# Kernel tuning notes

Measured on AMD Instinct MI355X. Metric: run time of the kernel, lower is better.

Reference implementation:

```python
import jax, jax.numpy as jnp
import numpy as np

B, C, H, W = 8, 256, 48, 48

def setup_inputs() -> dict:
    key = jax.random.key(0)
    ks = jax.random.split(key, 8)
    s = 1.0 / np.sqrt(C)  # conv2d default init scale (uniform fan_in)
    x = jax.random.normal(ks[0], (B, C, H, W), dtype=jnp.float32)
    y = jax.random.normal(ks[1], (B, C, H, W), dtype=jnp.float32)
    Wq = jax.random.uniform(ks[2], (C, C), jnp.float32, -s, s)
    bq = jax.random.uniform(ks[3], (C,), jnp.float32, -s, s)
    Wk = jax.random.uniform(ks[4], (C, C), jnp.float32, -s, s)
    bk = jax.random.uniform(ks[5], (C,), jnp.float32, -s, s)
    Wv = jax.random.uniform(ks[6], (C, C), jnp.float32, -s, s)
    bv = jax.random.uniform(ks[7], (C,), jnp.float32, -s, s)
    return {"x": x, "y": y, "Wq": Wq, "bq": bq, "Wk": Wk, "bk": bk, "Wv": Wv, "bv": bv}

def reference(x, y, Wq, bq, Wk, bk, Wv, bv):
    b, c, h, w = x.shape
    n = h * w
    # [B,C,H,W] -> tokens [B,N,C]
    xt = x.reshape(b, c, n).transpose(0, 2, 1)
    yt = y.reshape(b, c, n).transpose(0, 2, 1)
    # 1x1 convs == per-token linear projections
    q = xt @ Wq.T + bq  # [B,N,C]
    k = yt @ Wk.T + bk  # [B,N,C]
    v = yt @ Wv.T + bv  # [B,N,C]
    # unscaled QK^T softmax (module applies no 1/sqrt(d) scaling)
    scores = jnp.einsum('bnc,bmc->bnm', q, k)  # [B,N,N]
    attn = jax.nn.softmax(scores, axis=-1)
    out = jnp.einsum('bnm,bmc->bnc', attn, v)  # [B,N,C]
    return out.transpose(0, 2, 1).reshape(b, c, h, w)
```

## Files before the change

### kernel.cpp

```cpp
#include <hip/hip_runtime.h>
#include <stdint.h>

#define Bb 8
#define Cc 256
#define Nn 2304
#define PJT 18
#define QT 18
#define KSPLIT 3
#define TPS 24
#define L2E 1.44269504088896f
#define DEFER_THR 8.0f

#define AS1 __attribute__((address_space(1)))
#define AS3 __attribute__((address_space(3)))

typedef unsigned short u16;
typedef unsigned int u32;
typedef _Float16 h16;
typedef h16  h16x8 __attribute__((ext_vector_type(8)));
typedef u16  u16x8 __attribute__((ext_vector_type(8)));
typedef u16  u16x4 __attribute__((ext_vector_type(4)));
typedef u32  u32x4 __attribute__((ext_vector_type(4)));
typedef float f32x4 __attribute__((ext_vector_type(4)));
typedef float f32x2 __attribute__((ext_vector_type(2)));

static __device__ __forceinline__ u16 f2h(float f) {
  return __builtin_bit_cast(u16, (h16)f);
}
static __device__ __forceinline__ float h2f(u16 v) {
  return (float)__builtin_bit_cast(h16, v);
}
static __device__ __forceinline__ h16x8 ash(u16x8 v) {
  return __builtin_bit_cast(h16x8, v);
}
static __device__ __forceinline__ f32x4 mfma16(u16x8 a, u16x8 b, f32x4 c) {
  return __builtin_amdgcn_mfma_f32_16x16x32_f16(ash(a), ash(b), c, 0, 0, 0);
}
static __device__ __forceinline__ u32 pkf16(float a, float b) {
  return __builtin_bit_cast(u32, __builtin_amdgcn_cvt_pkrtz(a, b));
}

__global__ void prep_kernel(const float* __restrict__ Wq,
                            const float* __restrict__ Wk,
                            const float* __restrict__ Wv,
                            u16* __restrict__ Wf)
{
  const int tid = blockIdx.x * 256 + threadIdx.x;
  const int m   = tid >> 13;
  const int off = (tid & 8191) * 8;
  const float* src = (m == 0) ? Wq : (m == 1) ? Wk : Wv;
  const f32x4 a = *(const f32x4*)(src + off);
  const f32x4 c = *(const f32x4*)(src + off + 4);
  u16x8 o;
#pragma unroll
  for (int j = 0; j < 4; ++j) { o[j] = f2h(a[j]); o[j + 4] = f2h(c[j]); }
  *(u16x8*)(Wf + (size_t)m * 65536 + off) = o;
}

__global__ __launch_bounds__(256, 2) void proj_kernel(
    const float* __restrict__ x, const float* __restrict__ y,
    const u16* __restrict__ Wf,
    const float* __restrict__ bq, const float* __restrict__ bk,
    const float* __restrict__ bv,
    u16* __restrict__ Qf, u16* __restrict__ Kf, u16* __restrict__ Vf)
{
  __shared__ u16 sW[2][64 * 256];
  const int t    = threadIdx.x;
  const int b    = blockIdx.x;
  const int q0   = blockIdx.y * 128;
  const int z    = blockIdx.z;
  const int lane = t & 63;
  const int w    = t >> 6;
  const int quad = lane >> 4;
  const int l15  = lane & 15;

  const u16* WZ = Wf + (size_t)z * 65536;

  const int rbase = 2 * w + (lane >> 5);
  const int wcol  = ((lane & 31) ^ rbase) << 3;

  auto stage = [&](int rg, int buf) {
#pragma unroll
    for (int it = 0; it < 8; ++it) {
      __builtin_amdgcn_global_load_lds(
          (const AS1 void*)(WZ + (size_t)(rg * 64 + rbase + 8 * it) * 256 + wcol),
          (AS3 void*)&sW[buf][(w + 4 * it) * 512], 16, 0, 0);
    }
  };

  stage(0, 0);

  const float* src = (z == 0) ? x : y;
  u16x8 af[2][8];
#pragma unroll
  for (int g = 0; g < 2; ++g) {
    const int tok = q0 + g * 64 + w * 16 + l15;
#pragma unroll
    for (int kc = 0; kc < 8; ++kc) {
      const float* p = src + ((size_t)b * Cc + kc * 32 + quad * 8) * Nn + tok;
      float v[8];
#pragma unroll
      for (int j = 0; j < 8; ++j) v[j] = p[(size_t)j * Nn];
#pragma unroll
      for (int j = 0; j < 8; ++j) af[g][kc][j] = f2h(v[j]);
    }
  }

  f32x4 acc[2][16];
#pragma unroll
  for (int g = 0; g < 2; ++g)
#pragma unroll
    for (int i = 0; i < 16; ++i) acc[g][i] = (f32x4){0.f, 0.f, 0.f, 0.f};

  int cur = 0;
#pragma unroll 1
  for (int rg = 0; rg < 4; ++rg) {
    __builtin_amdgcn_s_waitcnt(0x0F70);
    __syncthreads();
    if (rg + 1 < 4) stage(rg + 1, cur ^ 1);
#pragma unroll
    for (int cbl = 0; cbl < 4; ++cbl) {
      const int rl = cbl * 16 + l15;
      f32x4 a0 = acc[0][rg * 4 + cbl];
      f32x4 a1 = acc[1][rg * 4 + cbl];
#pragma unroll
      for (int kc = 0; kc < 8; ++kc) {
        const u16x8 bf = *(const u16x8*)(sW[cur] + rl * 256 + (((kc * 4 + quad) ^ (rl & 7)) << 3));
        if (z < 2) {
          a0 = mfma16(af[0][kc], bf, a0);
          a1 = mfma16(af[1][kc], bf, a1);
        } else {
          a0 = mfma16(bf, af[0][kc], a0);
          a1 = mfma16(bf, af[1][kc], a1);
        }
      }
      acc[0][rg * 4 + cbl] = a0;
      acc[1][rg * 4 + cbl] = a1;
    }
    cur ^= 1;
  }

  u16* sT = &sW[0][0];
  if (z < 2) {
    const float* bias = (z == 0) ? bq : bk;
    u16* O = (z == 0) ? Qf : Kf;
#pragma unroll
    for (int g = 0; g < 2; ++g) {
      __syncthreads();
#pragma unroll
      for (int cb = 0; cb < 16; ++cb) {
        const int col = cb * 16 + l15;
        const float bs = bias[col];
#pragma unroll
        for (int r = 0; r < 4; ++r) {
          const int row = w * 16 + quad * 4 + r;
          sT[row * 256 + (col ^ ((row & 7) << 3))] = f2h(acc[g][cb][r] + bs);
        }
      }
      __syncthreads();
      const size_t ob = ((size_t)b * Nn + q0 + g * 64) * Cc;
#pragma unroll
      for (int i = 0; i < 8; ++i) {
        const int lin = i * 256 + t;
        const int row = lin >> 5, ch = lin & 31;
        const u16x8 v = *(const u16x8*)(sT + row * 256 + ((ch ^ (row & 7)) << 3));
        *(u16x8*)(O + ob + (size_t)lin * 8) = v;
      }
    }
  } else {
#pragma unroll
    for (int g = 0; g < 2; ++g) {
      __syncthreads();
#pragma unroll
      for (int cb = 0; cb < 16; ++cb) {
#pragma unroll
        for (int r = 0; r < 4; ++r) {
          const int c = cb * 16 + quad * 4 + r;
          const int col = w * 16 + l15;
          sT[c * 64 + (col ^ ((c & 7) << 3))] = f2h(acc[g][cb][r] + bv[c]);
        }
      }
      __syncthreads();
#pragma unroll
      for (int i = 0; i < 8; ++i) {
        const int lin = i * 256 + t;
        const int row = lin >> 3, g8 = lin & 7;
        const u16x8 v = *(const u16x8*)(sT + row * 64 + ((g8 ^ (row & 7)) << 3));
        *(u16x8*)(Vf + ((size_t)b * Cc + row) * Nn + q0 + g * 64 + g8 * 8) = v;
      }
    }
  }
}

__global__ __launch_bounds__(256, 2) void attn_kernel(
    const u16* __restrict__ Qf, const u16* __restrict__ Kf,
    const u16* __restrict__ Vf, u16* __restrict__ OpH,
    float* __restrict__ Ml)
{
  __shared__ u16 sK[2][32 * 256];
  __shared__ u16 sV[2][256 * 32];
  const int t    = threadIdx.x;
  const int b    = blockIdx.x;
  const int q0   = blockIdx.y * 128;
  const int sp   = blockIdx.z;
  const int lane = t & 63;
  const int w    = t >> 6;
  const int quad = lane >> 4;
  const int l15  = lane & 15;
  const int wq0  = q0 + w * 32;

  const u16* Kb = Kf + (size_t)b * Nn * Cc;
  const u16* Vb = Vf + (size_t)b * Cc * Nn;

  const int rbase = 2 * w + (lane >> 5);
  const int kcol  = ((lane & 31) ^ rbase) << 3;
  const int rb2 = rbase >> 2, rb3 = rbase & 3;
  int koff[4];
#pragma unroll
  for (int it = 0; it < 4; ++it) {
    const int key = (((rb2 + 2 * it) & 3) << 3) + rb3 + ((it >> 1) << 2);
    koff[it] = key * Cc + kcol;
  }
  const u16* Kt = Kb + (size_t)(sp * TPS * 32) * Cc;
  const int cV   = w * 16 + (lane >> 2);
  const int vcol = ((lane & 3) ^ ((cV >> 1) & 3)) << 3;
  const u16* vp0 = Vb + (size_t)cV * Nn + sp * TPS * 32 + vcol;

  auto stage = [&](int kb, int buf) {
#pragma unroll
    for (int it = 0; it < 4; ++it) {
      __builtin_amdgcn_global_load_lds(
          (const AS1 void*)(Kt + (size_t)kb * 32 * Cc + koff[it]),
          (AS3 void*)&sK[buf][(w + 4 * it) * 512], 16, 0, 0);
      __builtin_amdgcn_global_load_lds(
          (const AS1 void*)(vp0 + kb * 32 + (size_t)it * 64 * Nn),
          (AS3 void*)&sV[buf][(w + 4 * it) * 512], 16, 0, 0);
    }
  };

  stage(0, 0);

  u16x8 qf[2][8];
#pragma unroll
  for (int g = 0; g < 2; ++g) {
    const size_t qrow = ((size_t)b * Nn + wq0 + g * 16 + l15) * Cc;
#pragma unroll
    for (int kc = 0; kc < 8; ++kc)
      qf[g][kc] = *(const u16x8*)(Qf + qrow + kc * 32 + quad * 8);
  }

  f32x4 o[2][16];
#pragma unroll
  for (int g = 0; g < 2; ++g)
#pragma unroll
    for (int i = 0; i < 16; ++i) o[g][i] = (f32x4){0.f, 0.f, 0.f, 0.f};
  float mrow[2] = {-3e38f, -3e38f};
  float lrow[2] = {0.f, 0.f};

  const int vbase = l15 * 32 + ((quad ^ ((l15 >> 1) & 3)) << 3);

  int cur = 0;
#pragma unroll 1
  for (int kb = 0; kb < TPS; ++kb) {
    __builtin_amdgcn_s_waitcnt(0x0F70);
    __syncthreads();

    f32x4 s[2][2];
    s[0][0] = (f32x4){0.f, 0.f, 0.f, 0.f}; s[0][1] = s[0][0];
    s[1][0] = s[0][0];                      s[1][1] = s[0][0];
#pragma unroll
    for (int kc = 0; kc < 8; ++kc) {
      const int ch = ((kc * 4 + quad) ^ (l15 & 7)) << 3;
      const u16x8 k0 = *(const u16x8*)(sK[cur] + l15 * 256 + ch);
      const u16x8 k1 = *(const u16x8*)(sK[cur] + (16 + l15) * 256 + ch);
      s[0][0] = mfma16(k0, qf[0][kc], s[0][0]);
      s[0][1] = mfma16(k1, qf[0][kc], s[0][1]);
      s[1][0] = mfma16(k0, qf[1][kc], s[1][0]);
      s[1][1] = mfma16(k1, qf[1][kc], s[1][1]);
    }

    if (kb + 1 < TPS) stage(kb + 1, cur ^ 1);

    u16x8 pf[2];
    float al[2];
    int needany = 0;
#pragma unroll
    for (int g = 0; g < 2; ++g) {
      float mloc = fmaxf(
          fmaxf(fmaxf(s[g][0][0], s[g][0][1]), fmaxf(s[g][0][2], s[g][0][3])),
          fmaxf(fmaxf(s[g][1][0], s[g][1][1]), fmaxf(s[g][1][2], s[g][1][3])));
      mloc = fmaxf(mloc, __shfl_xor(mloc, 16, 64));
      mloc = fmaxf(mloc, __shfl_xor(mloc, 32, 64));
      const bool need = mloc > mrow[g] + DEFER_THR;
      const float mn  = need ? mloc : mrow[g];
      al[g] = need ? exp2f((mrow[g] - mn) * L2E) : 1.f;
      mrow[g] = mn;
      needany |= (int)need;

      float p[8];
      float sum = 0.f;
#pragma unroll
      for (int r = 0; r < 4; ++r) {
        p[r]     = exp2f((s[g][0][r] - mn) * L2E);
        p[4 + r] = exp2f((s[g][1][r] - mn) * L2E);
        sum += p[r] + p[4 + r];
      }
      sum += __shfl_xor(sum, 16, 64);
      sum += __shfl_xor(sum, 32, 64);
      lrow[g] = lrow[g] * al[g] + sum;

      u32x4 pw;
      pw[0] = pkf16(p[0], p[1]);
      pw[1] = pkf16(p[2], p[3]);
      pw[2] = pkf16(p[4], p[5]);
      pw[3] = pkf16(p[6], p[7]);
      pf[g] = __builtin_bit_cast(u16x8, pw);
    }

    if (__any(needany)) {
#pragma unroll
      for (int i = 0; i < 16; ++i) {
#pragma unroll
        for (int r = 0; r < 4; ++r) {
          o[0][i][r] *= al[0];
          o[1][i][r] *= al[1];
        }
      }
    }

#pragma unroll
    for (int cb = 0; cb < 16; ++cb) {
      const u16x8 vf = *(const u16x8*)(sV[cur] + cb * 512 + vbase);
      o[0][cb] = mfma16(vf, pf[0], o[0][cb]);
      o[1][cb] = mfma16(vf, pf[1], o[1][cb]);
    }

    cur ^= 1;
  }

  u16* Ob = OpH + ((size_t)sp * Bb + b) * (size_t)Cc * Nn;
#pragma unroll
  for (int g = 0; g < 2; ++g) {
    const float inv = 1.f / lrow[g];
    const int qn = wq0 + g * 16 + l15;
#pragma unroll
    for (int cb = 0; cb < 16; ++cb) {
#pragma unroll
      for (int r = 0; r < 4; ++r)
        Ob[(size_t)(cb * 16 + quad * 4 + r) * Nn + qn] = f2h(o[g][cb][r] * inv);
    }
  }
  if (lane < 16) {
    float* mlb = Ml + ((size_t)sp * Bb + b) * (size_t)Nn * 2;
#pragma unroll
    for (int g = 0; g < 2; ++g) {
      const int qn = wq0 + g * 16 + l15;
      *(f32x2*)(mlb + (size_t)qn * 2) = (f32x2){mrow[g], lrow[g]};
    }
  }
}

__global__ void merge_kernel(const u16* __restrict__ OpH,
                             const float* __restrict__ Ml,
                             float* __restrict__ out)
{
  const int idx = blockIdx.x * 256 + threadIdx.x;
  const int n4 = idx % 576;
  const int bc = idx / 576;
  const int b  = bc >> 8;
  const size_t obase = (size_t)bc * Nn + n4 * 4;

  float oh[KSPLIT][4], mv[KSPLIT][4], lv[KSPLIT][4];
#pragma unroll
  for (int s = 0; s < KSPLIT; ++s) {
    const u16x4 hv = *(const u16x4*)(OpH + ((size_t)s * Bb * Cc + bc) * Nn + n4 * 4);
#pragma unroll
    for (int j = 0; j < 4; ++j) oh[s][j] = h2f(hv[j]);
    const float* ml = Ml + ((size_t)s * Bb + b) * (size_t)Nn * 2 + n4 * 8;
    const f32x4 u0 = *(const f32x4*)ml;
    const f32x4 u1 = *(const f32x4*)(ml + 4);
#pragma unroll
    for (int j = 0; j < 4; ++j) {
      mv[s][j] = (j < 2) ? u0[j * 2]     : u1[(j - 2) * 2];
      lv[s][j] = (j < 2) ? u0[j * 2 + 1] : u1[(j - 2) * 2 + 1];
    }
  }

  f32x4 r;
#pragma unroll
  for (int j = 0; j < 4; ++j) {
    float m = mv[0][j];
#pragma unroll
    for (int s = 1; s < KSPLIT; ++s) m = fmaxf(m, mv[s][j]);
    float num = 0.f, den = 0.f;
#pragma unroll
    for (int s = 0; s < KSPLIT; ++s) {
      const float ws = lv[s][j] * exp2f((mv[s][j] - m) * L2E);
      num += oh[s][j] * ws;
      den += ws;
    }
    r[j] = num / den;
  }
  *(f32x4*)(out + obase) = r;
}

extern "C" void kernel_launch(void* const* d_in, const int* in_sizes, int n_in,
                              void* d_out, int out_size, void* d_ws, size_t ws_size,
                              hipStream_t stream) {
  const float* x  = (const float*)d_in[0];
  const float* y  = (const float*)d_in[1];
  const float* Wq = (const float*)d_in[2];
  const float* bq = (const float*)d_in[3];
  const float* Wk = (const float*)d_in[4];
  const float* bk = (const float*)d_in[5];
  const float* Wv = (const float*)d_in[6];
  const float* bv = (const float*)d_in[7];
  float* out = (float*)d_out;

  const size_t NC = (size_t)Bb * Nn * Cc;
  u16* Qf = (u16*)d_ws;
  u16* Kf = Qf + NC;
  u16* Vf = Kf + NC;
  u16* Wf = Vf + NC;
  u16* OpH = Wf + 3 * 65536;
  float* Ml = (float*)(OpH + (size_t)KSPLIT * NC);

  hipLaunchKernelGGL(prep_kernel, dim3(96), dim3(256), 0, stream,
                     Wq, Wk, Wv, Wf);
  hipLaunchKernelGGL(proj_kernel, dim3(Bb, PJT, 3), dim3(256), 0, stream,
                     x, y, Wf, bq, bk, bv, Qf, Kf, Vf);
  hipLaunchKernelGGL(attn_kernel, dim3(Bb, QT, KSPLIT), dim3(256), 0, stream,
                     Qf, Kf, Vf, OpH, Ml);
  hipLaunchKernelGGL(merge_kernel, dim3(4608), dim3(256), 0, stream,
                     OpH, Ml, out);
}
```

Baseline: 223.4 us.

## Pre-transpose x and y to token-major fp16 in the prep kernel

```diff
diff --git a/kernel.cpp b/kernel.cpp
--- a/kernel.cpp
+++ b/kernel.cpp
@@ -43,22 +43,62 @@
 __global__ void prep_kernel(const float* __restrict__ Wq,
                             const float* __restrict__ Wk,
                             const float* __restrict__ Wv,
-                            u16* __restrict__ Wf)
+                            const float* __restrict__ x,
+                            const float* __restrict__ y,
+                            u16* __restrict__ Wf,
+                            u16* __restrict__ Xt,
+                            u16* __restrict__ Yt)
 {
-  const int tid = blockIdx.x * 256 + threadIdx.x;
-  const int m   = tid >> 13;
-  const int off = (tid & 8191) * 8;
-  const float* src = (m == 0) ? Wq : (m == 1) ? Wk : Wv;
-  const f32x4 a = *(const f32x4*)(src + off);
-  const f32x4 c = *(const f32x4*)(src + off + 4);
-  u16x8 o;
-#pragma unroll
-  for (int j = 0; j < 4; ++j) { o[j] = f2h(a[j]); o[j + 4] = f2h(c[j]); }
-  *(u16x8*)(Wf + (size_t)m * 65536 + off) = o;
+  const int bid = blockIdx.x;
+  const int t   = threadIdx.x;
+  if (bid < 96) {
+    const int tid = bid * 256 + t;
+    const int m   = tid >> 13;
+    const int off = (tid & 8191) * 8;
+    const float* src = (m == 0) ? Wq : (m == 1) ? Wk : Wv;
+    const f32x4 a = *(const f32x4*)(src + off);
+    const f32x4 c = *(const f32x4*)(src + off + 4);
+    u16x8 o;
+#pragma unroll
+    for (int j = 0; j < 4; ++j) { o[j] = f2h(a[j]); o[j + 4] = f2h(c[j]); }
+    *(u16x8*)(Wf + (size_t)m * 65536 + off) = o;
+    return;
+  }
+  __shared__ u16 sT[64 * 64];
+  const int id2  = bid - 96;
+  const float* src = (id2 < 1152) ? x : y;
+  u16* dst         = (id2 < 1152) ? Xt : Yt;
+  const int id3  = id2 % 1152;
+  const int b    = id3 / 144;
+  const int rem  = id3 % 144;
+  const int tok0 = (rem >> 2) * 64;
+  const int c0   = (rem & 3) * 64;
+
+#pragma unroll
+  for (int i = 0; i < 4; ++i) {
+    const int id4 = i * 256 + t;
+    const int cl  = id4 >> 4;
+    const int t4  = id4 & 15;
+    const f32x4 v = *(const f32x4*)(src + ((size_t)b * Cc + c0 + cl) * Nn + tok0 + t4 * 4);
+#pragma unroll
+    for (int j = 0; j < 4; ++j) {
+      const int tok = t4 * 4 + j;
+      sT[tok * 64 + (cl ^ ((t4 & 7) << 3))] = f2h(v[j]);
+    }
+  }
+  __syncthreads();
+#pragma unroll
+  for (int i = 0; i < 2; ++i) {
+    const int id5 = i * 256 + t;
+    const int tok = id5 >> 3;
+    const int c8  = (id5 & 7) * 8;
+    const u16x8 vv = *(const u16x8*)(sT + tok * 64 + (c8 ^ (((tok >> 2) & 7) << 3)));
+    *(u16x8*)(dst + ((size_t)b * Nn + tok0 + tok) * Cc + c0 + c8) = vv;
+  }
 }
 
 __global__ __launch_bounds__(256, 2) void proj_kernel(
-    const float* __restrict__ x, const float* __restrict__ y,
+    const u16* __restrict__ Xt, const u16* __restrict__ Yt,
     const u16* __restrict__ Wf,
     const float* __restrict__ bq, const float* __restrict__ bk,
     const float* __restrict__ bv,
@@ -90,20 +130,14 @@
 
   stage(0, 0);
 
-  const float* src = (z == 0) ? x : y;
+  const u16* S = (z == 0) ? Xt : Yt;
   u16x8 af[2][8];
 #pragma unroll
   for (int g = 0; g < 2; ++g) {
-    const int tok = q0 + g * 64 + w * 16 + l15;
-#pragma unroll
-    for (int kc = 0; kc < 8; ++kc) {
-      const float* p = src + ((size_t)b * Cc + kc * 32 + quad * 8) * Nn + tok;
-      float v[8];
-#pragma unroll
-      for (int j = 0; j < 8; ++j) v[j] = p[(size_t)j * Nn];
-#pragma unroll
-      for (int j = 0; j < 8; ++j) af[g][kc][j] = f2h(v[j]);
-    }
+    const size_t row = ((size_t)b * Nn + q0 + g * 64 + w * 16 + l15) * Cc;
+#pragma unroll
+    for (int kc = 0; kc < 8; ++kc)
+      af[g][kc] = *(const u16x8*)(S + row + kc * 32 + quad * 8);
   }
 
   f32x4 acc[2][16];
@@ -424,11 +458,13 @@
   u16* Wf = Vf + NC;
   u16* OpH = Wf + 3 * 65536;
   float* Ml = (float*)(OpH + (size_t)KSPLIT * NC);
-
-  hipLaunchKernelGGL(prep_kernel, dim3(96), dim3(256), 0, stream,
-                     Wq, Wk, Wv, Wf);
+  u16* Xt = (u16*)(Ml + (size_t)KSPLIT * Bb * Nn * 2);
+  u16* Yt = Xt + NC;
+
+  hipLaunchKernelGGL(prep_kernel, dim3(2400), dim3(256), 0, stream,
+                     Wq, Wk, Wv, x, y, Wf, Xt, Yt);
   hipLaunchKernelGGL(proj_kernel, dim3(Bb, PJT, 3), dim3(256), 0, stream,
-                     x, y, Wf, bq, bk, bv, Qf, Kf, Vf);
+                     Xt, Yt, Wf, bq, bk, bv, Qf, Kf, Vf);
   hipLaunchKernelGGL(attn_kernel, dim3(Bb, QT, KSPLIT), dim3(256), 0, stream,
                      Qf, Kf, Vf, OpH, Ml);
   hipLaunchKernelGGL(merge_kernel, dim3(4608), dim3(256), 0, stream,
```

Result: no change. 221.5 us (-0.8%).
